# Kernel tuning notes

Measured on AMD Instinct MI355X. Metric: run time of the kernel, lower is better.

The kernel has to match this reference:

```python
import jax, jax.numpy as jnp
import numpy as np

# ---- constants from module defaults (n_transducers reduced 64->32) ----
ARC = 160          # transducer_arc_width
NTR = 32           # n_transducers
NMEAS = 256
NX = 360           # padded grid size
DX = 0.6
NSTEPS = 640       # nt
DT = 0.2
SIGMA = 12.0
TC = 3.2
FC = 1.0
NBC = 15
PAD = 73
C1, C2, C3 = -2.5, 4.0 / 3.0, -1.0 / 12.0

_thetas = np.linspace(0.0, 2.0 * np.pi, NMEAS + 1)[:-1]
_ti = np.floor(ARC * np.stack((np.cos(_thetas), np.sin(_thetas))) + (NX - 1) / 2).astype(np.int32)
MEAS_INDS = jnp.asarray(NX * _ti[0, :] + _ti[1, :])          # [256] flat grid indices
IN_INDS = MEAS_INDS[:: NMEAS // NTR]                         # [32] source-injection indices
_t = np.arange(NSTEPS) * DT
SOURCE = jnp.asarray((np.exp(-((_t - TC) ** 2) / (2.0 * SIGMA ** 2)) * np.sin(2.0 * np.pi * FC * _t)).astype(np.float32))


def get_abc(vp):
    # vp: [B, NX, NX] -> sponge damping profile, same overwrite order as torch code
    B = vp.shape[0]
    dimr = jnp.arange(NBC, dtype=vp.dtype)                   # [nbc]
    velmin = jnp.min(vp.reshape(B, -1), axis=-1)             # [B]
    a = (NBC - 1) * DX
    kappa = 3.0 * velmin * jnp.asarray(np.log(10000.0), vp.dtype) / (2.0 * a)
    d1 = kappa[:, None] * (dimr[None, :] * DX / a) ** 2      # [B, nbc]
    rev = d1[:, ::-1]
    damp = jnp.zeros_like(vp)
    damp = damp.at[:, :NBC, :].set(rev[:, :, None])
    damp = damp.at[:, -NBC:, :].set(d1[:, :, None])
    damp = damp.at[:, :, :NBC].set(rev[:, None, :])          # columns overwrite corners, as in torch
    damp = damp.at[:, :, -NBC:].set(d1[:, None, :])
    return damp


def _forward(v):
    v = jnp.pad(v[:, 0], ((0, 0), (PAD, PAD), (PAD, PAD)), constant_values=1.5)  # [B,360,360]
    B = v.shape[0]
    kappa = get_abc(v) * DT
    v2 = v * v
    alpha = v2 * (DT / DX) ** 2                              # [B,360,360]
    beta = (DT * DT) * v2.reshape(B, -1)[:, IN_INDS]         # [B,NTR]
    temp1 = 2.0 + 2.0 * C1 * alpha - kappa
    temp0 = 1.0 - kappa
    a_, t1_, t0_ = alpha[:, None], temp1[:, None], temp0[:, None]  # broadcast over transducer axis
    tx = jnp.arange(NTR)

    def step(carry, src_t):
        p0, p1 = carry                                        # each [B,NTR,360,360]
        lap = C2 * (jnp.roll(p1, 1, -2) + jnp.roll(p1, -1, -2) + jnp.roll(p1, 1, -1) + jnp.roll(p1, -1, -1)) \
            + C3 * (jnp.roll(p1, 2, -2) + jnp.roll(p1, -2, -2) + jnp.roll(p1, 2, -1) + jnp.roll(p1, -2, -1))
        p = a_ * lap + t1_ * p1 - t0_ * p0
        pf = p.reshape(B, NTR, NX * NX)
        pf = pf.at[:, tx, IN_INDS].add(beta * src_t)          # per-shot source injection
        m = pf[:, :, MEAS_INDS]                               # [B,NTR,NMEAS]
        return (p1, pf.reshape(B, NTR, NX, NX)), m

    z = jnp.zeros((B, NTR, NX, NX), dtype=v.dtype)
    _, meas = jax.lax.scan(step, (z, z), SOURCE)              # meas: [NSTEPS,B,NTR,NMEAS]
    return jnp.transpose(meas, (1, 2, 0, 3))                  # [B,NTR,NSTEPS,NMEAS]


def setup_inputs() -> dict:
    key = jax.random.key(0)
    v = jax.random.uniform(key, (1, 1, 214, 214), dtype=jnp.float32) + 1.0  # speeds ~[1,2]
    return {"v": v}


def reference(v):
    return _forward(v)
```

## Files before the change

### kernel.cpp

```cpp
#include <hip/hip_runtime.h>
#include <math.h>

#ifndef M_PI
#define M_PI 3.14159265358979323846
#endif

#define NXx   360
#define NXY   (NXx*NXx)
#define NTRc  32
#define NMEASc 256
#define NSTEPSc 640
#define NBCc  15
#define PADc  73
#define NVc   214

#define BROWS 45
#define NBANDS 8
#define NBLK  (NTRc*NBANDS)
#define NTHREADS 832
#define NGrow (NXx/4)
#define NSTRIPT 810
#define LDSROWS 49
#define LDSFLOATS (2*LDSROWS*NXx)
#define NSLOT 4
#define HALO_PER (NSLOT*4*NXx)

#define C2f   1.3333334f
#define C3f  (-0.083333336f)
#define ADX2  0.11111111f
#define DT2f  0.04f
#define DTf   0.2f
#define DXf   0.6f

typedef float f32x4 __attribute__((ext_vector_type(4)));

__device__ __forceinline__ void store4_sys(float* p, float4 v) {
    f32x4 vv; vv.x = v.x; vv.y = v.y; vv.z = v.z; vv.w = v.w;
    asm volatile("global_store_dwordx4 %0, %1, off sc0 sc1" :: "v"(p), "v"(vv) : "memory");
}
__device__ __forceinline__ float4 load4_sys(const float* p) {
    f32x4 r;
    asm volatile("global_load_dwordx4 %0, %1, off sc0 sc1\n\ts_waitcnt vmcnt(0)"
                 : "=&v"(r) : "v"(p) : "memory");
    return make_float4(r.x, r.y, r.z, r.w);
}
__device__ __forceinline__ void storei_sys(int* p, int v) {
    asm volatile("global_store_dword %0, %1, off sc0 sc1" :: "v"(p), "v"(v) : "memory");
}
__device__ __forceinline__ int loadi_sys(const int* p) {
    int r;
    asm volatile("global_load_dword %0, %1, off sc0 sc1\n\ts_waitcnt vmcnt(0)"
                 : "=&v"(r) : "v"(p) : "memory");
    return r;
}
__device__ __forceinline__ void drain_vm() {
    asm volatile("s_waitcnt vmcnt(0)" ::: "memory");
}

__global__ void velmin_kernel(const float* __restrict__ v, float* __restrict__ velmin) {
    __shared__ float s[256];
    float m = 1.5f;
    for (int i = threadIdx.x; i < NVc*NVc; i += 256) m = fminf(m, v[i]);
    s[threadIdx.x] = m;
    __syncthreads();
    for (int o = 128; o > 0; o >>= 1) {
        if (threadIdx.x < o) s[threadIdx.x] = fminf(s[threadIdx.x], s[threadIdx.x+o]);
        __syncthreads();
    }
    if (threadIdx.x == 0) *velmin = s[0];
}

__global__ void coef_kernel(const float* __restrict__ v, const float* __restrict__ velmin_p,
                            float* __restrict__ alpha, float* __restrict__ kap) {
    int idx = blockIdx.x*256 + threadIdx.x;
    if (idx >= NXY) return;
    int i = idx / NXx, j = idx - i*NXx;
    float vc = 1.5f;
    if (i >= PADc && i < PADc+NVc && j >= PADc && j < PADc+NVc)
        vc = v[(i-PADc)*NVc + (j-PADc)];
    float v2 = vc*vc;
    float al = v2 * ADX2;
    float velmin = *velmin_p;
    const float a = (float)((NBCc-1)*0.6);
    float ks = 3.0f*velmin*9.2103405f/(2.0f*a);
    float damp = 0.0f;
    int k = -1;
    if (j >= NXx-NBCc)      k = j-(NXx-NBCc);
    else if (j < NBCc)      k = NBCc-1-j;
    else if (i >= NXx-NBCc) k = i-(NXx-NBCc);
    else if (i < NBCc)      k = NBCc-1-i;
    if (k >= 0) { float r = (float)k*DXf/a; damp = ks*r*r; }
    alpha[idx] = al;
    kap[idx]   = damp*DTf;
}

__global__ void beta_kernel(const float* __restrict__ v, const int* __restrict__ in_inds,
                            float* __restrict__ beta) {
    int tr = threadIdx.x;
    if (tr >= NTRc) return;
    int idx = in_inds[tr];
    int i = idx / NXx, j = idx - i*NXx;
    float vc = 1.5f;
    if (i >= PADc && i < PADc+NVc && j >= PADc && j < PADc+NVc)
        vc = v[(i-PADc)*NVc + (j-PADc)];
    beta[tr] = DT2f*vc*vc;
}

__global__ __launch_bounds__(NTHREADS, 4) void persist_kernel(
    const float* __restrict__ alpha, const float* __restrict__ kap,
    const float* __restrict__ beta, const float* __restrict__ src,
    const int* __restrict__ meas_inds, const int* __restrict__ in_inds,
    int* flags, float* haloG, float* __restrict__ out)
{
    extern __shared__ float lds[];
    const int tid  = threadIdx.x;
    const int b    = blockIdx.x;
    const int tr   = b >> 3, band = b & 7;
    const int band0 = band*BROWS;
    const int up = (tr<<3) | ((band+7)&7);
    const int dn = (tr<<3) | ((band+1)&7);

    float* buf0 = lds;
    float* buf1 = lds + LDSROWS*NXx;

    for (int i = tid; i < LDSFLOATS; i += NTHREADS) lds[i] = 0.0f;

    const float betaV = beta[tr];
    const int sCell = in_inds[tr];
    const int sr = sCell/NXx, sc = sCell - sr*NXx;

    const bool isStrip = (tid < NSTRIPT);
    const int s  = isStrip ? (tid/NGrow) : 0;
    const int jg = isStrip ? (tid - s*NGrow) : 0;
    const int r0 = 5*s;
    const bool isEdge = isStrip && (s == 0 || s == 8);
    const int jgm = (jg==0) ? NGrow-1 : jg-1;
    const int jgp = (jg==NGrow-1) ? 0 : jg+1;

    float4 Ar[5], Kr[5];
    int qrow = -1, qcomp = 0;
    if (isStrip) {
#pragma unroll
        for (int k = 0; k < 5; ++k) {
            int gi = (band0 + r0 + k)*NXx + jg*4;
            Ar[k] = *(const float4*)(alpha + gi);
            Kr[k] = *(const float4*)(kap + gi);
        }
        if (sr >= band0+r0 && sr < band0+r0+5 && (sc>>2) == jg) {
            qrow = sr - (band0+r0); qcomp = sc & 3;
        }
    } else {
#pragma unroll
        for (int k = 0; k < 5; ++k) { Ar[k] = make_float4(0,0,0,0); Kr[k] = Ar[k]; }
    }

    bool mOwn = false; int mOff = 0;
    float* outP = out + ((size_t)tr*NSTEPSc)*NMEASc + tid;
    if (tid < NMEASc) {
        int mi = meas_inds[tid]; int row = mi/NXx, col = mi - row*NXx;
        if (row >= band0 && row < band0+BROWS) { mOwn = true; mOff = (row-band0+2)*NXx + col; }
    }

    float* myHalo = haloG + (size_t)b*HALO_PER;
    float* upHalo = haloG + (size_t)up*HALO_PER;
    float* dnHalo = haloG + (size_t)dn*HALO_PER;

    __syncthreads();

#define STRIP_COMPUTE(DOHALO) { \
    const int base = r0*NGrow + jg; \
    float4 cm2 = cur4[base]; \
    float4 cm1 = cur4[base+NGrow]; \
    float4 cc0 = cur4[base+2*NGrow]; \
    float4 cp1 = cur4[base+3*NGrow]; \
    float4 cp2 = cur4[base+4*NGrow]; \
    _Pragma("unroll") \
    for (int k = 0; k < 5; ++k) { \
        const int ci = base + (2+k)*NGrow; \
        float4 Lv = cur4[ci - jg + jgm]; \
        float4 Rv = cur4[ci - jg + jgp]; \
        float4 Pp = nxt4[ci]; \
        float4 po; \
        { float lap = C2f*(cm1.x+cp1.x+Lv.w+cc0.y) + C3f*(cm2.x+cp2.x+Lv.z+cc0.z); \
          float t1v = 2.0f + 2.0f*(-2.5f)*Ar[k].x - Kr[k].x; float t0v = 1.0f - Kr[k].x; \
          po.x = Ar[k].x*lap + t1v*cc0.x - t0v*Pp.x; } \
        { float lap = C2f*(cm1.y+cp1.y+cc0.x+cc0.z) + C3f*(cm2.y+cp2.y+Lv.w+cc0.w); \
          float t1v = 2.0f + 2.0f*(-2.5f)*Ar[k].y - Kr[k].y; float t0v = 1.0f - Kr[k].y; \
          po.y = Ar[k].y*lap + t1v*cc0.y - t0v*Pp.y; } \
        { float lap = C2f*(cm1.z+cp1.z+cc0.y+cc0.w) + C3f*(cm2.z+cp2.z+cc0.x+Rv.x); \
          float t1v = 2.0f + 2.0f*(-2.5f)*Ar[k].z - Kr[k].z; float t0v = 1.0f - Kr[k].z; \
          po.z = Ar[k].z*lap + t1v*cc0.z - t0v*Pp.z; } \
        { float lap = C2f*(cm1.w+cp1.w+cc0.z+Rv.x) + C3f*(cm2.w+cp2.w+cc0.y+Rv.y); \
          float t1v = 2.0f + 2.0f*(-2.5f)*Ar[k].w - Kr[k].w; float t0v = 1.0f - Kr[k].w; \
          po.w = Ar[k].w*lap + t1v*cc0.w - t0v*Pp.w; } \
        if (k == qrow) { float add = betaV*srcT; \
            po.x += (qcomp==0)?add:0.0f; po.y += (qcomp==1)?add:0.0f; \
            po.z += (qcomp==2)?add:0.0f; po.w += (qcomp==3)?add:0.0f; } \
        nxt4[ci] = po; \
        if (DOHALO) { \
            if (s == 0 && k < 2) store4_sys(myHalo + hsOff + k*NXx + jg*4, po); \
            if (s == 8 && k >= 3) store4_sys(myHalo + hsOff + (k-1)*NXx + jg*4, po); \
        } \
        cm2 = cm1; cm1 = cc0; cc0 = cp1; cp1 = cp2; \
        if (k < 4) cp2 = cur4[base + (5+k)*NGrow]; \
    } }

    for (int t = 0; t < NSTEPSc; ++t) {
        const int slot = t & 1;
        const int hs   = (t+1) & 3;
        const int hsOff = hs*4*NXx;
        float* cur = (slot == 0) ? buf0 : buf1;
        float* nxt = (slot == 0) ? buf1 : buf0;
        const float4* cur4 = (const float4*)cur;
        float4* nxt4 = (float4*)nxt;
        const float srcT = src[t];

        if (isEdge) {
            STRIP_COMPUTE(1)
            drain_vm();
        }
        __syncthreads();
        if (tid == 0) storei_sys(flags + b, t + 1);

        if (isStrip && !isEdge) {
            STRIP_COMPUTE(0)
        }

        if (tid == 0) {
            int g = 0;
            while (loadi_sys(flags + up) <= t)
                { __builtin_amdgcn_s_sleep(1); if (++g > 200000) break; }
        }
        if (tid == 64) {
            int g = 0;
            while (loadi_sys(flags + dn) <= t)
                { __builtin_amdgcn_s_sleep(1); if (++g > 200000) break; }
        }
        __syncthreads();

        if (tid < 4*NGrow) {
            int rr = tid / NGrow, jgq = tid - rr*NGrow;
            const float* sp = (rr < 2) ? (upHalo + (hsOff + (2+rr)*NXx) + jgq*4)
                                       : (dnHalo + (hsOff + (rr-2)*NXx) + jgq*4);
            float4 hv = load4_sys(sp);
            int ldr = (rr < 2) ? rr : (45 + rr);
            *(float4*)(nxt + ldr*NXx + jgq*4) = hv;
        }

        if (mOwn) outP[(size_t)t*NMEASc] = nxt[mOff];

        __syncthreads();
    }
#undef STRIP_COMPUTE
}

extern "C" void kernel_launch(void* const* d_in, const int* in_sizes, int n_in,
                              void* d_out, int out_size, void* d_ws, size_t ws_size,
                              hipStream_t stream) {
    const float* v = (const float*)d_in[0];
    float* out = (float*)d_out;

    float* haloG  = (float*)d_ws;
    float* alpha  = haloG + (size_t)NBLK*HALO_PER;
    float* kap    = alpha + NXY;
    float* beta   = kap + NXY;
    float* velmin = beta + NTRc;
    float* src_d  = velmin + 1;
    int*   meas_d = (int*)(src_d + NSTEPSc);
    int*   in_d   = meas_d + NMEASc;
    int*   flags  = in_d + NTRc;

    static int   h_tab[NMEASc + NTRc];
    static float h_src[NSTEPSc];
    {
        const double step = 2.0*M_PI/256.0;
        for (int k = 0; k < NMEASc; ++k) {
            double th = (double)k * step;
            int ti0 = (int)floor(160.0*cos(th) + 179.5);
            int ti1 = (int)floor(160.0*sin(th) + 179.5);
            h_tab[k] = NXx*ti0 + ti1;
        }
        for (int r = 0; r < NTRc; ++r) h_tab[NMEASc + r] = h_tab[r*(NMEASc/NTRc)];
        for (int t = 0; t < NSTEPSc; ++t) {
            double tt = (double)t * 0.2;
            double d  = tt - 3.2;
            double e  = exp(-(d*d) / 288.0);
            double s  = sin(6.283185307179586 * tt);
            h_src[t] = (float)(e * s);
        }
    }
    (void)hipMemcpyAsync(meas_d, h_tab, sizeof(int)*(NMEASc+NTRc), hipMemcpyHostToDevice, stream);
    (void)hipMemcpyAsync(src_d, h_src, sizeof(float)*NSTEPSc, hipMemcpyHostToDevice, stream);
    (void)hipMemsetAsync(haloG, 0, sizeof(float)*(size_t)NBLK*HALO_PER, stream);
    (void)hipMemsetAsync(flags, 0, sizeof(int)*NBLK, stream);

    velmin_kernel<<<1, 256, 0, stream>>>(v, velmin);
    coef_kernel<<<(NXY+255)/256, 256, 0, stream>>>(v, velmin, alpha, kap);
    beta_kernel<<<1, 64, 0, stream>>>(v, in_d, beta);

    (void)hipFuncSetAttribute((const void*)persist_kernel,
                        hipFuncAttributeMaxDynamicSharedMemorySize, LDSFLOATS*4);

    persist_kernel<<<NBLK, NTHREADS, LDSFLOATS*4, stream>>>(
        alpha, kap, beta, src_d, meas_d, in_d, flags, haloG, out);
}
```

Before: 2.469 ms.

## Restructure halo exchange: edge waves sync via LDS counter, keep p0 in registers

Edge strips are now placed in dedicated wavefronts. They publish their halo flag through an LDS atomic counter instead of a block barrier, then poll the neighbour flags and load halos themselves, which removes one of the two per-step __syncthreads. The previous-step field is kept in registers (Pv) instead of being read back from LDS. The bottom edge strip is computed in reverse order so its halo rows are finished first. Measurement output is deferred by one step, and the halo memset is dropped. The thread count grows to 896, and the spin loops on workgroup-scope atomics add a risk of hazards or extra register pressure.

```diff
diff --git a/kernel.cpp b/kernel.cpp
--- a/kernel.cpp
+++ b/kernel.cpp
@@ -17,9 +17,8 @@
 #define BROWS 45
 #define NBANDS 8
 #define NBLK  (NTRc*NBANDS)
-#define NTHREADS 832
+#define NTHREADS 896
 #define NGrow (NXx/4)
-#define NSTRIPT 810
 #define LDSROWS 49
 #define LDSFLOATS (2*LDSROWS*NXx)
 #define NSLOT 4
@@ -38,11 +37,15 @@
     f32x4 vv; vv.x = v.x; vv.y = v.y; vv.z = v.z; vv.w = v.w;
     asm volatile("global_store_dwordx4 %0, %1, off sc0 sc1" :: "v"(p), "v"(vv) : "memory");
 }
-__device__ __forceinline__ float4 load4_sys(const float* p) {
-    f32x4 r;
-    asm volatile("global_load_dwordx4 %0, %1, off sc0 sc1\n\ts_waitcnt vmcnt(0)"
-                 : "=&v"(r) : "v"(p) : "memory");
-    return make_float4(r.x, r.y, r.z, r.w);
+__device__ __forceinline__ void load4x2_sys(const float* p0, const float* p1,
+                                            float4& a, float4& b) {
+    f32x4 r0, r1;
+    asm volatile("global_load_dwordx4 %0, %2, off sc0 sc1\n\t"
+                 "global_load_dwordx4 %1, %3, off sc0 sc1\n\t"
+                 "s_waitcnt vmcnt(0)"
+                 : "=&v"(r0), "=&v"(r1) : "v"(p0), "v"(p1) : "memory");
+    a = make_float4(r0.x, r0.y, r0.z, r0.w);
+    b = make_float4(r1.x, r1.y, r1.z, r1.w);
 }
 __device__ __forceinline__ void storei_sys(int* p, int v) {
     asm volatile("global_store_dword %0, %1, off sc0 sc1" :: "v"(p), "v"(v) : "memory");
@@ -113,6 +116,7 @@
     int* flags, float* haloG, float* __restrict__ out)
 {
     extern __shared__ float lds[];
+    unsigned* cnt = (unsigned*)(lds + LDSFLOATS);
     const int tid  = threadIdx.x;
     const int b    = blockIdx.x;
     const int tr   = b >> 3, band = b & 7;
@@ -123,21 +127,24 @@
     float* buf0 = lds;
     float* buf1 = lds + LDSROWS*NXx;
 
-    for (int i = tid; i < LDSFLOATS; i += NTHREADS) lds[i] = 0.0f;
+    for (int i = tid; i < LDSFLOATS + 4; i += NTHREADS) lds[i] = 0.0f;
 
     const float betaV = beta[tr];
     const int sCell = in_inds[tr];
-    const int sr = sCell/NXx, sc = sCell - sr*NXx;
-
-    const bool isStrip = (tid < NSTRIPT);
-    const int s  = isStrip ? (tid/NGrow) : 0;
-    const int jg = isStrip ? (tid - s*NGrow) : 0;
-    const int r0 = 5*s;
-    const bool isEdge = isStrip && (s == 0 || s == 8);
+    const int sr = sCell/NXx, scc = sCell - sr*NXx;
+
+    int sIdx = -1, jg = 0;
+    if      (tid < 90)                { sIdx = 0; jg = tid; }
+    else if (tid >= 128 && tid < 218) { sIdx = 8; jg = tid - 128; }
+    else if (tid >= 256 && tid < 886) { int idx = tid - 256; sIdx = 1 + idx/90; jg = idx - 90*(idx/90); }
+    const bool isStrip = (sIdx >= 0);
+    const bool isTop   = (sIdx == 0);
+    const bool isEdge  = (sIdx == 0) || (sIdx == 8);
+    const int r0 = 5*sIdx;
     const int jgm = (jg==0) ? NGrow-1 : jg-1;
     const int jgp = (jg==NGrow-1) ? 0 : jg+1;
 
-    float4 Ar[5], Kr[5];
+    float4 Ar[5], Kr[5], Pv[5];
     int qrow = -1, qcomp = 0;
     if (isStrip) {
 #pragma unroll
@@ -145,20 +152,24 @@
             int gi = (band0 + r0 + k)*NXx + jg*4;
             Ar[k] = *(const float4*)(alpha + gi);
             Kr[k] = *(const float4*)(kap + gi);
-        }
-        if (sr >= band0+r0 && sr < band0+r0+5 && (sc>>2) == jg) {
-            qrow = sr - (band0+r0); qcomp = sc & 3;
-        }
+            Pv[k] = make_float4(0.f, 0.f, 0.f, 0.f);
+        }
+        int sb = sr - band0;
+        if (sb >= r0 && sb < r0+5 && (scc>>2) == jg) { qrow = sb - r0; qcomp = scc & 3; }
     } else {
 #pragma unroll
-        for (int k = 0; k < 5; ++k) { Ar[k] = make_float4(0,0,0,0); Kr[k] = Ar[k]; }
+        for (int k = 0; k < 5; ++k) { Ar[k] = make_float4(0,0,0,0); Kr[k] = Ar[k]; Pv[k] = Ar[k]; }
     }
 
     bool mOwn = false; int mOff = 0;
-    float* outP = out + ((size_t)tr*NSTEPSc)*NMEASc + tid;
-    if (tid < NMEASc) {
-        int mi = meas_inds[tid]; int row = mi/NXx, col = mi - row*NXx;
-        if (row >= band0 && row < band0+BROWS) { mOwn = true; mOff = (row-band0+2)*NXx + col; }
+    float* outP = out;
+    if (tid >= 256 && tid < 512) {
+        int mIdx = tid - 256;
+        int mi = meas_inds[mIdx]; int row = mi/NXx, col = mi - row*NXx;
+        if (row >= band0 && row < band0+BROWS) {
+            mOwn = true; mOff = (row-band0+2)*NXx + col;
+            outP = out + ((size_t)tr*NSTEPSc)*NMEASc + mIdx;
+        }
     }
 
     float* myHalo = haloG + (size_t)b*HALO_PER;
@@ -167,7 +178,29 @@
 
     __syncthreads();
 
-#define STRIP_COMPUTE(DOHALO) { \
+#define CELL_BODY(KIDX) \
+    float4 Lv = cur4[ci - jg + jgm]; \
+    float4 Rv = cur4[ci - jg + jgp]; \
+    float4 po; \
+    { float lap = C2f*(cm1.x+cp1.x+Lv.w+cc0.y) + C3f*(cm2.x+cp2.x+Lv.z+cc0.z); \
+      float t1v = 2.0f + 2.0f*(-2.5f)*Ar[KIDX].x - Kr[KIDX].x; float t0v = 1.0f - Kr[KIDX].x; \
+      po.x = Ar[KIDX].x*lap + t1v*cc0.x - t0v*Pv[KIDX].x; } \
+    { float lap = C2f*(cm1.y+cp1.y+cc0.x+cc0.z) + C3f*(cm2.y+cp2.y+Lv.w+cc0.w); \
+      float t1v = 2.0f + 2.0f*(-2.5f)*Ar[KIDX].y - Kr[KIDX].y; float t0v = 1.0f - Kr[KIDX].y; \
+      po.y = Ar[KIDX].y*lap + t1v*cc0.y - t0v*Pv[KIDX].y; } \
+    { float lap = C2f*(cm1.z+cp1.z+cc0.y+cc0.w) + C3f*(cm2.z+cp2.z+cc0.x+Rv.x); \
+      float t1v = 2.0f + 2.0f*(-2.5f)*Ar[KIDX].z - Kr[KIDX].z; float t0v = 1.0f - Kr[KIDX].z; \
+      po.z = Ar[KIDX].z*lap + t1v*cc0.z - t0v*Pv[KIDX].z; } \
+    { float lap = C2f*(cm1.w+cp1.w+cc0.z+Rv.x) + C3f*(cm2.w+cp2.w+cc0.y+Rv.y); \
+      float t1v = 2.0f + 2.0f*(-2.5f)*Ar[KIDX].w - Kr[KIDX].w; float t0v = 1.0f - Kr[KIDX].w; \
+      po.w = Ar[KIDX].w*lap + t1v*cc0.w - t0v*Pv[KIDX].w; } \
+    if (KIDX == qrow) { float add = betaV*srcT; \
+        po.x += (qcomp==0)?add:0.0f; po.y += (qcomp==1)?add:0.0f; \
+        po.z += (qcomp==2)?add:0.0f; po.w += (qcomp==3)?add:0.0f; } \
+    nxt4[ci] = po; \
+    Pv[KIDX] = cc0;
+
+#define STRIP_FWD(DOHALO) { \
     const int base = r0*NGrow + jg; \
     float4 cm2 = cur4[base]; \
     float4 cm1 = cur4[base+NGrow]; \
@@ -177,32 +210,27 @@
     _Pragma("unroll") \
     for (int k = 0; k < 5; ++k) { \
         const int ci = base + (2+k)*NGrow; \
-        float4 Lv = cur4[ci - jg + jgm]; \
-        float4 Rv = cur4[ci - jg + jgp]; \
-        float4 Pp = nxt4[ci]; \
-        float4 po; \
-        { float lap = C2f*(cm1.x+cp1.x+Lv.w+cc0.y) + C3f*(cm2.x+cp2.x+Lv.z+cc0.z); \
-          float t1v = 2.0f + 2.0f*(-2.5f)*Ar[k].x - Kr[k].x; float t0v = 1.0f - Kr[k].x; \
-          po.x = Ar[k].x*lap + t1v*cc0.x - t0v*Pp.x; } \
-        { float lap = C2f*(cm1.y+cp1.y+cc0.x+cc0.z) + C3f*(cm2.y+cp2.y+Lv.w+cc0.w); \
-          float t1v = 2.0f + 2.0f*(-2.5f)*Ar[k].y - Kr[k].y; float t0v = 1.0f - Kr[k].y; \
-          po.y = Ar[k].y*lap + t1v*cc0.y - t0v*Pp.y; } \
-        { float lap = C2f*(cm1.z+cp1.z+cc0.y+cc0.w) + C3f*(cm2.z+cp2.z+cc0.x+Rv.x); \
-          float t1v = 2.0f + 2.0f*(-2.5f)*Ar[k].z - Kr[k].z; float t0v = 1.0f - Kr[k].z; \
-          po.z = Ar[k].z*lap + t1v*cc0.z - t0v*Pp.z; } \
-        { float lap = C2f*(cm1.w+cp1.w+cc0.z+Rv.x) + C3f*(cm2.w+cp2.w+cc0.y+Rv.y); \
-          float t1v = 2.0f + 2.0f*(-2.5f)*Ar[k].w - Kr[k].w; float t0v = 1.0f - Kr[k].w; \
-          po.w = Ar[k].w*lap + t1v*cc0.w - t0v*Pp.w; } \
-        if (k == qrow) { float add = betaV*srcT; \
-            po.x += (qcomp==0)?add:0.0f; po.y += (qcomp==1)?add:0.0f; \
-            po.z += (qcomp==2)?add:0.0f; po.w += (qcomp==3)?add:0.0f; } \
-        nxt4[ci] = po; \
-        if (DOHALO) { \
-            if (s == 0 && k < 2) store4_sys(myHalo + hsOff + k*NXx + jg*4, po); \
-            if (s == 8 && k >= 3) store4_sys(myHalo + hsOff + (k-1)*NXx + jg*4, po); \
-        } \
+        CELL_BODY(k) \
+        if (DOHALO && k < 2) store4_sys(myHalo + hsOff + k*NXx + jg*4, po); \
         cm2 = cm1; cm1 = cc0; cc0 = cp1; cp1 = cp2; \
         if (k < 4) cp2 = cur4[base + (5+k)*NGrow]; \
+    } }
+
+#define STRIP_REV(DOHALO) { \
+    const int base = r0*NGrow + jg; \
+    float4 cp2 = cur4[base+8*NGrow]; \
+    float4 cp1 = cur4[base+7*NGrow]; \
+    float4 cc0 = cur4[base+6*NGrow]; \
+    float4 cm1 = cur4[base+5*NGrow]; \
+    float4 cm2 = cur4[base+4*NGrow]; \
+    _Pragma("unroll") \
+    for (int kk = 0; kk < 5; ++kk) { \
+        const int k = 4 - kk; \
+        const int ci = base + (2+k)*NGrow; \
+        CELL_BODY(k) \
+        if (DOHALO && k >= 3) store4_sys(myHalo + hsOff + (k-1)*NXx + jg*4, po); \
+        cp2 = cp1; cp1 = cc0; cc0 = cm1; cm1 = cm2; \
+        if (kk < 4) cm2 = cur4[base + (k-1)*NGrow]; \
     } }
 
     for (int t = 0; t < NSTEPSc; ++t) {
@@ -215,43 +243,49 @@
         float4* nxt4 = (float4*)nxt;
         const float srcT = src[t];
 
+        if (mOwn && t > 0) outP[(size_t)(t-1)*NMEASc] = cur[mOff];
+
         if (isEdge) {
-            STRIP_COMPUTE(1)
+            if (isTop) { STRIP_FWD(true) } else { STRIP_REV(true) }
             drain_vm();
-        }
+            if ((tid & 63) == 0) atomicAdd(cnt, 1u);
+            if (tid == 64) {
+                int g = 0;
+                while (__hip_atomic_load(cnt, __ATOMIC_RELAXED, __HIP_MEMORY_SCOPE_WORKGROUP)
+                       < 4u*(unsigned)(t+1)) { if (++g > 20000000) break; }
+                storei_sys(flags + b, t + 1);
+            }
+            if (tid == 0 || tid == 64) {
+                int g = 0;
+                while (loadi_sys(flags + up) <= t)
+                    { __builtin_amdgcn_s_sleep(1); if (++g > 2000000) break; }
+            }
+            if (tid == 128 || tid == 192) {
+                int g = 0;
+                while (loadi_sys(flags + dn) <= t)
+                    { __builtin_amdgcn_s_sleep(1); if (++g > 2000000) break; }
+            }
+            float4 ha, hb;
+            if (isTop) {
+                load4x2_sys(upHalo + hsOff + 2*NXx + jg*4, upHalo + hsOff + 3*NXx + jg*4, ha, hb);
+                *(float4*)(nxt + jg*4)       = ha;
+                *(float4*)(nxt + NXx + jg*4) = hb;
+            } else {
+                load4x2_sys(dnHalo + hsOff + jg*4, dnHalo + hsOff + NXx + jg*4, ha, hb);
+                *(float4*)(nxt + 47*NXx + jg*4) = ha;
+                *(float4*)(nxt + 48*NXx + jg*4) = hb;
+            }
+        } else if (isStrip) {
+            STRIP_FWD(false)
+        }
+
         __syncthreads();
-        if (tid == 0) storei_sys(flags + b, t + 1);
-
-        if (isStrip && !isEdge) {
-            STRIP_COMPUTE(0)
-        }
-
-        if (tid == 0) {
-            int g = 0;
-            while (loadi_sys(flags + up) <= t)
-                { __builtin_amdgcn_s_sleep(1); if (++g > 200000) break; }
-        }
-        if (tid == 64) {
-            int g = 0;
-            while (loadi_sys(flags + dn) <= t)
-                { __builtin_amdgcn_s_sleep(1); if (++g > 200000) break; }
-        }
-        __syncthreads();
-
-        if (tid < 4*NGrow) {
-            int rr = tid / NGrow, jgq = tid - rr*NGrow;
-            const float* sp = (rr < 2) ? (upHalo + (hsOff + (2+rr)*NXx) + jgq*4)
-                                       : (dnHalo + (hsOff + (rr-2)*NXx) + jgq*4);
-            float4 hv = load4_sys(sp);
-            int ldr = (rr < 2) ? rr : (45 + rr);
-            *(float4*)(nxt + ldr*NXx + jgq*4) = hv;
-        }
-
-        if (mOwn) outP[(size_t)t*NMEASc] = nxt[mOff];
-
-        __syncthreads();
-    }
-#undef STRIP_COMPUTE
+    }
+
+    if (mOwn) outP[(size_t)(NSTEPSc-1)*NMEASc] = buf0[mOff];
+#undef STRIP_FWD
+#undef STRIP_REV
+#undef CELL_BODY
 }
 
 extern "C" void kernel_launch(void* const* d_in, const int* in_sizes, int n_in,
@@ -291,7 +325,6 @@
     }
     (void)hipMemcpyAsync(meas_d, h_tab, sizeof(int)*(NMEASc+NTRc), hipMemcpyHostToDevice, stream);
     (void)hipMemcpyAsync(src_d, h_src, sizeof(float)*NSTEPSc, hipMemcpyHostToDevice, stream);
-    (void)hipMemsetAsync(haloG, 0, sizeof(float)*(size_t)NBLK*HALO_PER, stream);
     (void)hipMemsetAsync(flags, 0, sizeof(int)*NBLK, stream);
 
     velmin_kernel<<<1, 256, 0, stream>>>(v, velmin);
@@ -299,8 +332,8 @@
     beta_kernel<<<1, 64, 0, stream>>>(v, in_d, beta);
 
     (void)hipFuncSetAttribute((const void*)persist_kernel,
-                        hipFuncAttributeMaxDynamicSharedMemorySize, LDSFLOATS*4);
-
-    persist_kernel<<<NBLK, NTHREADS, LDSFLOATS*4, stream>>>(
+                        hipFuncAttributeMaxDynamicSharedMemorySize, (LDSFLOATS+4)*4);
+
+    persist_kernel<<<NBLK, NTHREADS, (LDSFLOATS+4)*4, stream>>>(
         alpha, kap, beta, src_d, meas_d, in_d, flags, haloG, out);
 }
```

Result: slower. 4.059 ms (+64.4%).
